# Kernel tuning notes

Measured on AMD Instinct MI355X. Metric: run time of the kernel, lower is better.

The kernel has to match this reference:

```python
import jax, jax.numpy as jnp
import numpy as np

N_EMBD = 512
N_HEADS = 8
N_KV_HEADS = 2
HEAD_DIM = N_EMBD // N_HEADS  # 64
ROPE_BASE = 1000000.0
B, T = 2, 4096


def _rotate_half(x):
    h = x.shape[-1] // 2
    return jnp.concatenate([-x[..., h:], x[..., :h]], axis=-1)


def _build_rope(head_dim, seq_len, base, dtype):
    inv_freq = 1.0 / base ** (jnp.arange(0, head_dim, 2, dtype=jnp.float32) / head_dim)
    t = jnp.arange(seq_len, dtype=jnp.float32)
    freqs = jnp.outer(t, inv_freq)            # [T, head_dim/2]
    emb = jnp.concatenate([freqs, freqs], axis=-1)  # [T, head_dim]
    return emb.astype(dtype), None  # placeholder, cos/sin computed by caller


def setup_inputs() -> dict:
    key = jax.random.key(0)
    ks = jax.random.split(key, 8)
    s_in = 1.0 / np.sqrt(N_EMBD)
    x = jax.random.normal(ks[0], (B, T, N_EMBD), dtype=jnp.float32)
    Wq = jax.random.normal(ks[1], (N_EMBD, N_HEADS * HEAD_DIM), dtype=jnp.float32) * s_in
    bq = jnp.zeros((N_HEADS * HEAD_DIM,), dtype=jnp.float32)
    Wk = jax.random.normal(ks[2], (N_EMBD, N_KV_HEADS * HEAD_DIM), dtype=jnp.float32) * s_in
    bk = jnp.zeros((N_KV_HEADS * HEAD_DIM,), dtype=jnp.float32)
    Wv = jax.random.normal(ks[3], (N_EMBD, N_KV_HEADS * HEAD_DIM), dtype=jnp.float32) * s_in
    bv = jnp.zeros((N_KV_HEADS * HEAD_DIM,), dtype=jnp.float32)
    Wo = jax.random.normal(ks[4], (N_HEADS * HEAD_DIM, N_EMBD), dtype=jnp.float32) * s_in
    return {"x": x, "Wq": Wq, "bq": bq, "Wk": Wk, "bk": bk, "Wv": Wv, "bv": bv, "Wo": Wo}


def reference(x, Wq, bq, Wk, bk, Wv, bv, Wo):
    Bx, Tx, _ = x.shape
    scale = HEAD_DIM ** -0.5
    q = (x @ Wq + bq).reshape(Bx, Tx, N_HEADS, HEAD_DIM).transpose(0, 2, 1, 3)      # [B,H,T,D]
    k = (x @ Wk + bk).reshape(Bx, Tx, N_KV_HEADS, HEAD_DIM).transpose(0, 2, 1, 3)   # [B,Hkv,T,D]
    v = (x @ Wv + bv).reshape(Bx, Tx, N_KV_HEADS, HEAD_DIM).transpose(0, 2, 1, 3)

    # RoPE (built in fp32 then cast, matching torch impl)
    inv_freq = 1.0 / ROPE_BASE ** (jnp.arange(0, HEAD_DIM, 2, dtype=jnp.float32) / HEAD_DIM)
    t = jnp.arange(Tx, dtype=jnp.float32)
    freqs = jnp.outer(t, inv_freq)
    emb = jnp.concatenate([freqs, freqs], axis=-1)          # [T, D]
    cos = jnp.cos(emb).astype(x.dtype)[None, None, :, :]    # broadcast over B,H
    sin = jnp.sin(emb).astype(x.dtype)[None, None, :, :]
    q = q * cos + _rotate_half(q) * sin
    k = k * cos + _rotate_half(k) * sin

    rep = N_HEADS // N_KV_HEADS
    k = jnp.repeat(k, rep, axis=1)   # repeat_interleave on head dim
    v = jnp.repeat(v, rep, axis=1)

    attn = jnp.einsum("bhtd,bhsd->bhts", q, k) * scale      # [B,H,T,T]
    causal = jnp.tril(jnp.ones((Tx, Tx), dtype=bool))
    attn = jnp.where(causal, attn, jnp.finfo(attn.dtype).min)
    attn = jax.nn.softmax(attn, axis=-1)
    out = jnp.einsum("bhts,bhsd->bhtd", attn, v)            # [B,H,T,D]
    out = out.transpose(0, 2, 1, 3).reshape(Bx, Tx, N_HEADS * HEAD_DIM)
    return out @ Wo
```

## Files before the change

kernel.cpp:

```cpp
#include <hip/hip_runtime.h>

typedef unsigned short u16;
typedef unsigned int u32;
typedef __bf16 bf16x8_t __attribute__((ext_vector_type(8)));
typedef float f32x4_t __attribute__((ext_vector_type(4)));
typedef float f32x16_t __attribute__((ext_vector_type(16)));

#define T_SEQ 4096
#define EMB 512
#define NH 8
#define NKV 2
#define HD 64

__device__ __forceinline__ float bf2f(u16 h) {
    union { unsigned u; float f; } x; x.u = ((unsigned)h) << 16; return x.f;
}
__device__ __forceinline__ u16 f2bf(float f) {
    union { float f; unsigned u; } x; x.f = f;
    unsigned r = x.u + 0x7FFFu + ((x.u >> 16) & 1u);
    return (u16)(r >> 16);
}

__global__ void transpose_kernel(const float* __restrict__ W, u16* __restrict__ WT,
                                 int K, int N) {
    int i = blockIdx.x * 256 + threadIdx.x;
    if (i < K * N) {
        int n = i / K;
        int k = i - n * K;
        WT[i] = f2bf(W[(size_t)k * N + n]);
    }
}

__global__ void cvt_kernel(const float* __restrict__ in, u16* __restrict__ out, int n4) {
    int i = blockIdx.x * 256 + threadIdx.x;
    if (i < n4) {
        float4 v = *reinterpret_cast<const float4*>(in + (size_t)i * 4);
        u16 o[4] = { f2bf(v.x), f2bf(v.y), f2bf(v.z), f2bf(v.w) };
        *reinterpret_cast<uint2*>(out + (size_t)i * 4) = *reinterpret_cast<uint2*>(o);
    }
}

__global__ void rope_table_kernel(float* __restrict__ cost, float* __restrict__ sint) {
    int i = blockIdx.x * 256 + threadIdx.x;
    int t = i >> 5, j = i & 31;
    double invf = pow(1.0e6, -(double)j / 32.0);
    double ang = (double)t * invf;
    cost[i] = (float)cos(ang);
    sint[i] = (float)sin(ang);
}

template <int EPI>
__global__ __launch_bounds__(256)
void gemm_kernel(const u16* __restrict__ A, const u16* __restrict__ Bt, int K,
                 float* __restrict__ C, int N,
                 const float* __restrict__ bq, const float* __restrict__ bk,
                 const float* __restrict__ bv,
                 const float* __restrict__ cost, const float* __restrict__ sint,
                 u16* __restrict__ qw, u16* __restrict__ kw, u16* __restrict__ vt)
{
    __shared__ __align__(16) u16 As[128][72];
    __shared__ __align__(16) u16 Bs[128][72];

    const int tid  = threadIdx.x;
    const int lane = tid & 63, wave = tid >> 6;
    const int wr = wave >> 1, wc = wave & 1;
    const int tm = blockIdx.x, tn = blockIdx.y;
    const int lrow = lane & 15, lgrp = lane >> 4;

    f32x4_t acc[4][4];
#pragma unroll
    for (int i = 0; i < 4; ++i)
#pragma unroll
        for (int j = 0; j < 4; ++j) acc[i][j] = (f32x4_t){0.f, 0.f, 0.f, 0.f};

    for (int k0 = 0; k0 < K; k0 += 64) {
        __syncthreads();
        {
            const int r0 = tid >> 3;
            const int ko = (tid & 7) * 8;
#pragma unroll
            for (int rr = 0; rr < 4; ++rr) {
                int row = r0 + rr * 32;
                uint4 va = *reinterpret_cast<const uint4*>(A + (size_t)(tm * 128 + row) * K + k0 + ko);
                *reinterpret_cast<uint4*>(&As[row][ko]) = va;
                uint4 vb = *reinterpret_cast<const uint4*>(Bt + (size_t)(tn * 128 + row) * K + k0 + ko);
                *reinterpret_cast<uint4*>(&Bs[row][ko]) = vb;
            }
        }
        __syncthreads();
#pragma unroll
        for (int kc = 0; kc < 2; ++kc) {
            bf16x8_t af[4], bf[4];
#pragma unroll
            for (int mb = 0; mb < 4; ++mb)
                af[mb] = *reinterpret_cast<const bf16x8_t*>(&As[wr * 64 + mb * 16 + lrow][kc * 32 + lgrp * 8]);
#pragma unroll
            for (int nb = 0; nb < 4; ++nb)
                bf[nb] = *reinterpret_cast<const bf16x8_t*>(&Bs[wc * 64 + nb * 16 + lrow][kc * 32 + lgrp * 8]);
#pragma unroll
            for (int mb = 0; mb < 4; ++mb)
#pragma unroll
                for (int nb = 0; nb < 4; ++nb)
                    acc[mb][nb] = __builtin_amdgcn_mfma_f32_16x16x32_bf16(af[mb], bf[nb], acc[mb][nb], 0, 0, 0);
        }
    }

    if (EPI == 0) {
#pragma unroll
        for (int mb = 0; mb < 4; ++mb)
#pragma unroll
            for (int nb = 0; nb < 4; ++nb)
#pragma unroll
                for (int r = 0; r < 4; ++r) {
                    int row = tm * 128 + wr * 64 + mb * 16 + lgrp * 4 + r;
                    int col = tn * 128 + wc * 64 + nb * 16 + lrow;
                    C[(size_t)row * N + col] = acc[mb][nb][r];
                }
    } else {
        const float QSC = 0.125f * 1.44269504088896f;
#pragma unroll
        for (int mb = 0; mb < 4; ++mb)
#pragma unroll
            for (int r = 0; r < 4; ++r) {
                int grow = tm * 128 + wr * 64 + mb * 16 + lgrp * 4 + r;
                int b = grow >> 12, t = grow & 4095;
#pragma unroll
                for (int nb = 0; nb < 2; ++nb) {
                    int n = tn * 128 + wc * 64 + nb * 16 + lrow;
                    int j = n & 63;
                    float c0 = acc[mb][nb][r];
                    float c1 = acc[mb][nb + 2][r];
                    if (n < 512) {
                        c0 += bq[n]; c1 += bq[n + 32];
                        float cs = cost[t * 32 + j], sn = sint[t * 32 + j];
                        float r0 = (c0 * cs - c1 * sn) * QSC;
                        float r1 = (c1 * cs + c0 * sn) * QSC;
                        int h = n >> 6;
                        size_t base = ((size_t)(b * NH + h) * T_SEQ + t) * HD;
                        qw[base + j]      = f2bf(r0);
                        qw[base + j + 32] = f2bf(r1);
                    } else if (n < 640) {
                        int nn = n - 512;
                        c0 += bk[nn]; c1 += bk[nn + 32];
                        float cs = cost[t * 32 + j], sn = sint[t * 32 + j];
                        float r0 = c0 * cs - c1 * sn;
                        float r1 = c1 * cs + c0 * sn;
                        int hk2 = nn >> 6;
                        size_t base = ((size_t)(b * NKV + hk2) * T_SEQ + t) * HD;
                        kw[base + j]      = f2bf(r0);
                        kw[base + j + 32] = f2bf(r1);
                    } else {
                        int nn = n - 640;
                        c0 += bv[nn]; c1 += bv[nn + 32];
                        int hv = nn >> 6;
                        size_t base = (size_t)(b * NKV + hv) * HD * T_SEQ;
                        vt[base + (size_t)j * T_SEQ + t]        = f2bf(c0);
                        vt[base + (size_t)(j + 32) * T_SEQ + t] = f2bf(c1);
                    }
                }
            }
    }
}

__global__ __launch_bounds__(256)
void attn_kernel(const u16* __restrict__ qw, const u16* __restrict__ kw,
                 const u16* __restrict__ vt, u16* __restrict__ po0,
                 u16* __restrict__ po12, float* __restrict__ lb)
{
    __shared__ __align__(16) u16 Ks[2][64][64];
    __shared__ __align__(16) u16 Vs[2][64][64];

    int gid = blockIdx.x;
    int qt = 31, nt, nc;
    for (;;) {
        nt = 2 * qt + 2;
        nc = (nt + 21) / 22;
        int g = nc * 16;
        if (gid < g) break;
        gid -= g; --qt;
    }
    const int bh = gid / nc;
    const int ck = gid - bh * nc;
    const int b = bh >> 3, h = bh & 7, hk = h >> 2;
    const int kt0 = ck * nt / nc;
    const int kt1 = (ck + 1) * nt / nc;

    const int tid = threadIdx.x, lane = tid & 63, wave = tid >> 6;
    const int lid = lane & 31, hi = lane >> 5;
    const int q0 = qt * 128 + wave * 32;

    const u16* kbase  = kw + (size_t)(b * NKV + hk) * T_SEQ * HD;
    const u16* vtbase = vt + (size_t)(b * NKV + hk) * HD * T_SEQ;

    const int ss = tid >> 3;
    const int sg = tid & 7;
    const int swz = (sg ^ (ss & 7)) << 3;

    bf16x8_t qf[4];
    {
        const u16* qrow = qw + ((size_t)(b * NH + h) * T_SEQ + q0 + lid) * HD + 8 * hi;
#pragma unroll
        for (int t = 0; t < 4; ++t)
            qf[t] = *reinterpret_cast<const bf16x8_t*>(qrow + 16 * t);
    }

    f32x16_t o0, o1;
#pragma unroll
    for (int i = 0; i < 16; ++i) { o0[i] = 0.f; o1[i] = 0.f; }
    const float M_FIX = 16.0f;
    float l = 0.f;

    {
        const int s2 = kt0 * 64;
        uint4 ka  = *reinterpret_cast<const uint4*>(kbase + (size_t)(s2 + ss) * HD + sg * 8);
        uint4 kb2 = *reinterpret_cast<const uint4*>(kbase + (size_t)(s2 + ss + 32) * HD + sg * 8);
        uint4 va  = *reinterpret_cast<const uint4*>(vtbase + (size_t)ss * T_SEQ + s2 + sg * 8);
        uint4 vb2 = *reinterpret_cast<const uint4*>(vtbase + (size_t)(ss + 32) * T_SEQ + s2 + sg * 8);
        *reinterpret_cast<uint4*>(&Ks[0][ss][swz]) = ka;
        *reinterpret_cast<uint4*>(&Ks[0][ss + 32][swz]) = kb2;
        *reinterpret_cast<uint4*>(&Vs[0][ss][swz]) = va;
        *reinterpret_cast<uint4*>(&Vs[0][ss + 32][swz]) = vb2;
    }
    __syncthreads();

    for (int kt = kt0; kt < kt1; ++kt) {
        const int cur = (kt - kt0) & 1, nxt = cur ^ 1;
        const bool pre = (kt + 1 < kt1);

        uint4 kr0, kr1, vr0, vr1;
        if (pre) {
            const int s2 = (kt + 1) * 64;
            kr0 = *reinterpret_cast<const uint4*>(kbase + (size_t)(s2 + ss) * HD + sg * 8);
            kr1 = *reinterpret_cast<const uint4*>(kbase + (size_t)(s2 + ss + 32) * HD + sg * 8);
            vr0 = *reinterpret_cast<const uint4*>(vtbase + (size_t)ss * T_SEQ + s2 + sg * 8);
            vr1 = *reinterpret_cast<const uint4*>(vtbase + (size_t)(ss + 32) * T_SEQ + s2 + sg * 8);
        }

        if (kt * 64 <= q0 + 31) {
            const bool full = (kt * 64 + 32 <= q0 + 31);
            const bool mreq = (kt * 64 + 63 > q0);

            f32x16_t s0, s1;
#pragma unroll
            for (int i = 0; i < 16; ++i) { s0[i] = 0.f; s1[i] = 0.f; }
            __builtin_amdgcn_s_setprio(1);
#pragma unroll
            for (int t = 0; t < 4; ++t) {
                const int g = ((2 * t + hi) ^ (lid & 7)) << 3;
                bf16x8_t ka = *reinterpret_cast<const bf16x8_t*>(&Ks[cur][lid][g]);
                s0 = __builtin_amdgcn_mfma_f32_32x32x16_bf16(ka, qf[t], s0, 0, 0, 0);
                if (full) {
                    bf16x8_t kb2 = *reinterpret_cast<const bf16x8_t*>(&Ks[cur][lid + 32][g]);
                    s1 = __builtin_amdgcn_mfma_f32_32x32x16_bf16(kb2, qf[t], s1, 0, 0, 0);
                }
            }
            __builtin_amdgcn_s_setprio(0);

            if (mreq) {
                const int qg = q0 + lid;
                const int kvb = kt * 64 + 4 * hi;
#pragma unroll
                for (int r = 0; r < 16; ++r) {
                    int kv = kvb + (r & 3) + 8 * (r >> 2);
                    if (kv > qg) s0[r] = -1e30f;
                    if (full && kv + 32 > qg) s1[r] = -1e30f;
                }
            }

#pragma unroll
            for (int r = 0; r < 16; ++r) s0[r] = exp2f(s0[r] - M_FIX);
            if (full) {
#pragma unroll
                for (int r = 0; r < 16; ++r) s1[r] = exp2f(s1[r] - M_FIX);
            }

            {
                float rs = 0.f;
#pragma unroll
                for (int q4 = 0; q4 < 4; ++q4)
                    rs += (s0[4 * q4] + s0[4 * q4 + 1]) + (s0[4 * q4 + 2] + s0[4 * q4 + 3]);
                if (full) {
#pragma unroll
                    for (int q4 = 0; q4 < 4; ++q4)
                        rs += (s1[4 * q4] + s1[4 * q4 + 1]) + (s1[4 * q4 + 2] + s1[4 * q4 + 3]);
                }
                rs += __shfl_xor(rs, 32);
                l += rs;
            }

            bf16x8_t pa[4];
            {
                u32 pw[8], pe[8];
                uint4 f0, f1;
#pragma unroll
                for (int c = 0; c < 4; ++c) {
                    asm("v_cvt_pk_bf16_f32 %0, %1, %2" : "=v"(pw[2 * c])     : "v"(s0[4 * c]),     "v"(s0[4 * c + 1]));
                    asm("v_cvt_pk_bf16_f32 %0, %1, %2" : "=v"(pw[2 * c + 1]) : "v"(s0[4 * c + 2]), "v"(s0[4 * c + 3]));
                }
#pragma unroll
                for (int i = 0; i < 8; ++i) pe[i] = (u32)__shfl_xor((int)pw[i], 32);
                f0.x = hi ? pe[2] : pw[0]; f0.y = hi ? pe[3] : pw[1];
                f0.z = hi ? pw[2] : pe[0]; f0.w = hi ? pw[3] : pe[1];
                f1.x = hi ? pe[6] : pw[4]; f1.y = hi ? pe[7] : pw[5];
                f1.z = hi ? pw[6] : pe[4]; f1.w = hi ? pw[7] : pe[5];
                pa[0] = __builtin_bit_cast(bf16x8_t, f0);
                pa[1] = __builtin_bit_cast(bf16x8_t, f1);
                if (full) {
#pragma unroll
                    for (int c = 0; c < 4; ++c) {
                        asm("v_cvt_pk_bf16_f32 %0, %1, %2" : "=v"(pw[2 * c])     : "v"(s1[4 * c]),     "v"(s1[4 * c + 1]));
                        asm("v_cvt_pk_bf16_f32 %0, %1, %2" : "=v"(pw[2 * c + 1]) : "v"(s1[4 * c + 2]), "v"(s1[4 * c + 3]));
                    }
#pragma unroll
                    for (int i = 0; i < 8; ++i) pe[i] = (u32)__shfl_xor((int)pw[i], 32);
                    f0.x = hi ? pe[2] : pw[0]; f0.y = hi ? pe[3] : pw[1];
                    f0.z = hi ? pw[2] : pe[0]; f0.w = hi ? pw[3] : pe[1];
                    f1.x = hi ? pe[6] : pw[4]; f1.y = hi ? pe[7] : pw[5];
                    f1.z = hi ? pw[6] : pe[4]; f1.w = hi ? pw[7] : pe[5];
                    pa[2] = __builtin_bit_cast(bf16x8_t, f0);
                    pa[3] = __builtin_bit_cast(bf16x8_t, f1);
                }
            }

            __builtin_amdgcn_s_setprio(1);
            const int ns = full ? 4 : 2;
#pragma unroll
            for (int s = 0; s < 4; ++s) {
                if (s >= ns) break;
                const int g = ((2 * s + hi) ^ (lid & 7)) << 3;
                bf16x8_t v0f = *reinterpret_cast<const bf16x8_t*>(&Vs[cur][lid][g]);
                bf16x8_t v1f = *reinterpret_cast<const bf16x8_t*>(&Vs[cur][lid + 32][g]);
                o0 = __builtin_amdgcn_mfma_f32_32x32x16_bf16(pa[s], v0f, o0, 0, 0, 0);
                o1 = __builtin_amdgcn_mfma_f32_32x32x16_bf16(pa[s], v1f, o1, 0, 0, 0);
            }
            __builtin_amdgcn_s_setprio(0);
        }

        if (pre) {
            *reinterpret_cast<uint4*>(&Ks[nxt][ss][swz]) = kr0;
            *reinterpret_cast<uint4*>(&Ks[nxt][ss + 32][swz]) = kr1;
            *reinterpret_cast<uint4*>(&Vs[nxt][ss][swz]) = vr0;
            *reinterpret_cast<uint4*>(&Vs[nxt][ss + 32][swz]) = vr1;
            __syncthreads();
        }
    }

    {
        u16* pob = (ck == 0) ? po0 : (po12 + (size_t)(ck - 1) * 4194304);
        const int rowb = (bh * 32 + qt) * 128 + wave * 32;
#pragma unroll
        for (int r = 0; r < 16; ++r) {
            int qr = (r & 3) + 8 * (r >> 2) + 4 * hi;
            size_t base = (size_t)(rowb + qr) * HD;
            pob[base + lid]      = f2bf(o0[r]);
            pob[base + lid + 32] = f2bf(o1[r]);
        }
        if (hi == 0)
            lb[(size_t)ck * 65536 + rowb + lid] = l;
    }
}

__global__ __launch_bounds__(256)
void combine_kernel(const u16* __restrict__ po0, const u16* __restrict__ po12,
                    const float* __restrict__ lb, u16* __restrict__ ao)
{
    int id = blockIdx.x * 256 + threadIdx.x;
    int row = id >> 3, oct = id & 7;
    int bhqt = row >> 7, qrow = row & 127;
    int bh = bhqt >> 5, qt = bhqt & 31;
    int b = bh >> 3, h = bh & 7;
    int t = qt * 128 + qrow;
    int nc = (2 * qt + 2 + 21) / 22;

    float lsum = lb[row];
    if (nc > 1) lsum += lb[65536 + row];
    if (nc > 2) lsum += lb[131072 + row];
    float inv = 1.0f / lsum;

    float acc[8];
    {
        uint4 a = *reinterpret_cast<const uint4*>(po0 + (size_t)row * HD + oct * 8);
        const u16* pa = reinterpret_cast<const u16*>(&a);
#pragma unroll
        for (int j = 0; j < 8; ++j) acc[j] = bf2f(pa[j]);
    }
    if (nc > 1) {
        uint4 a = *reinterpret_cast<const uint4*>(po12 + (size_t)row * HD + oct * 8);
        const u16* pa = reinterpret_cast<const u16*>(&a);
#pragma unroll
        for (int j = 0; j < 8; ++j) acc[j] += bf2f(pa[j]);
    }
    if (nc > 2) {
        uint4 a = *reinterpret_cast<const uint4*>(po12 + 4194304 + (size_t)row * HD + oct * 8);
        const u16* pa = reinterpret_cast<const u16*>(&a);
#pragma unroll
        for (int j = 0; j < 8; ++j) acc[j] += bf2f(pa[j]);
    }

    u16 outv[8];
#pragma unroll
    for (int j = 0; j < 8; ++j) outv[j] = f2bf(acc[j] * inv);
    size_t base = ((size_t)(b * T_SEQ) + t) * EMB + h * HD + oct * 8;
    *reinterpret_cast<uint2*>(ao + base)     = *reinterpret_cast<uint2*>(&outv[0]);
    *reinterpret_cast<uint2*>(ao + base + 4) = *reinterpret_cast<uint2*>(&outv[4]);
}

extern "C" void kernel_launch(void* const* d_in, const int* in_sizes, int n_in,
                              void* d_out, int out_size, void* d_ws, size_t ws_size,
                              hipStream_t stream)
{
    const float* x  = (const float*)d_in[0];
    const float* Wq = (const float*)d_in[1];
    const float* bq = (const float*)d_in[2];
    const float* Wk = (const float*)d_in[3];
    const float* bk = (const float*)d_in[4];
    const float* Wv = (const float*)d_in[5];
    const float* bv = (const float*)d_in[6];
    const float* Wo = (const float*)d_in[7];
    float* out = (float*)d_out;

    char* ws = (char*)d_ws;
    u16*   WqkvT = (u16*)(ws);
    u16*   WoT   = (u16*)(ws + 786432);
    float* cost  = (float*)(ws + 1310720);
    float* sint  = (float*)(ws + 1835008);
    u16*   xbf   = (u16*)(ws + 2359296);
    u16*   qw    = (u16*)(ws + 10747904);
    u16*   kw    = (u16*)(ws + 19136512);
    u16*   vt    = (u16*)(ws + 21233664);
    u16*   ao    = (u16*)(ws + 23330816);
    u16*   po0   = xbf;
    u16*   po12  = (u16*)(ws + 31719424);
    float* lb    = (float*)(ws + 48496640);

    transpose_kernel<<<(512 * 512 + 255) / 256, 256, 0, stream>>>(Wq, WqkvT, 512, 512);
    transpose_kernel<<<(512 * 128 + 255) / 256, 256, 0, stream>>>(Wk, WqkvT + 512 * 512, 512, 128);
    transpose_kernel<<<(512 * 128 + 255) / 256, 256, 0, stream>>>(Wv, WqkvT + 640 * 512, 512, 128);
    transpose_kernel<<<(512 * 512 + 255) / 256, 256, 0, stream>>>(Wo, WoT, 512, 512);
    cvt_kernel<<<(2 * T_SEQ * EMB / 4 + 255) / 256, 256, 0, stream>>>(x, xbf, 2 * T_SEQ * EMB / 4);
    rope_table_kernel<<<(T_SEQ * 32) / 256, 256, 0, stream>>>(cost, sint);

    dim3 gp(64, 6);
    gemm_kernel<1><<<gp, 256, 0, stream>>>(xbf, WqkvT, 512, nullptr, 768,
                                           bq, bk, bv, cost, sint, qw, kw, vt);

    attn_kernel<<<1008, 256, 0, stream>>>(qw, kw, vt, po0, po12, lb);

    combine_kernel<<<65536 * 8 / 256, 256, 0, stream>>>(po0, po12, lb, ao);

    dim3 go(64, 4);
    gemm_kernel<0><<<go, 256, 0, stream>>>(ao, WoT, 512, out, 512,
                                           nullptr, nullptr, nullptr, nullptr, nullptr,
                                           nullptr, nullptr, nullptr);
}
```

Baseline: 161.3 us.

## Interleave head index in block mapping and use permlane32 swap for P repack

```diff
diff --git a/kernel.cpp b/kernel.cpp
--- a/kernel.cpp
+++ b/kernel.cpp
@@ -170,21 +170,20 @@
     __shared__ __align__(16) u16 Ks[2][64][64];
     __shared__ __align__(16) u16 Vs[2][64][64];
 
-    int gid = blockIdx.x;
-    int qt = 31, nt, nc;
+    const int hdix = blockIdx.x & 15;
+    int s = blockIdx.x >> 4;
+    int qt = 31, nc;
     for (;;) {
-        nt = 2 * qt + 2;
-        nc = (nt + 21) / 22;
-        int g = nc * 16;
-        if (gid < g) break;
-        gid -= g; --qt;
-    }
-    const int bh = gid / nc;
-    const int ck = gid - bh * nc;
-    const int b = bh >> 3, h = bh & 7, hk = h >> 2;
+        nc = (2 * qt + 23) / 22;
+        if (s < nc) break;
+        s -= nc; --qt;
+    }
+    const int ck = s;
+    const int nt = 2 * qt + 2;
     const int kt0 = ck * nt / nc;
     const int kt1 = (ck + 1) * nt / nc;
 
+    const int b = hdix >> 3, h = hdix & 7, hk = h >> 2;
     const int tid = threadIdx.x, lane = tid & 63, wave = tid >> 6;
     const int lid = lane & 31, hi = lane >> 5;
     const int q0 = qt * 128 + wave * 32;
@@ -204,9 +203,9 @@
             qf[t] = *reinterpret_cast<const bf16x8_t*>(qrow + 16 * t);
     }
 
-    f32x16_t o0, o1;
-#pragma unroll
-    for (int i = 0; i < 16; ++i) { o0[i] = 0.f; o1[i] = 0.f; }
+    f32x16_t o0, o1, z16;
+#pragma unroll
+    for (int i = 0; i < 16; ++i) { o0[i] = 0.f; o1[i] = 0.f; z16[i] = 0.f; }
     const float M_FIX = 16.0f;
     float l = 0.f;
 
@@ -241,17 +240,15 @@
             const bool mreq = (kt * 64 + 63 > q0);
 
             f32x16_t s0, s1;
-#pragma unroll
-            for (int i = 0; i < 16; ++i) { s0[i] = 0.f; s1[i] = 0.f; }
             __builtin_amdgcn_s_setprio(1);
 #pragma unroll
             for (int t = 0; t < 4; ++t) {
                 const int g = ((2 * t + hi) ^ (lid & 7)) << 3;
                 bf16x8_t ka = *reinterpret_cast<const bf16x8_t*>(&Ks[cur][lid][g]);
-                s0 = __builtin_amdgcn_mfma_f32_32x32x16_bf16(ka, qf[t], s0, 0, 0, 0);
+                s0 = __builtin_amdgcn_mfma_f32_32x32x16_bf16(ka, qf[t], (t == 0) ? z16 : s0, 0, 0, 0);
                 if (full) {
                     bf16x8_t kb2 = *reinterpret_cast<const bf16x8_t*>(&Ks[cur][lid + 32][g]);
-                    s1 = __builtin_amdgcn_mfma_f32_32x32x16_bf16(kb2, qf[t], s1, 0, 0, 0);
+                    s1 = __builtin_amdgcn_mfma_f32_32x32x16_bf16(kb2, qf[t], (t == 0) ? z16 : s1, 0, 0, 0);
                 }
             }
             __builtin_amdgcn_s_setprio(0);
@@ -290,19 +287,18 @@
 
             bf16x8_t pa[4];
             {
-                u32 pw[8], pe[8];
-                uint4 f0, f1;
+                u32 pw[8];
 #pragma unroll
                 for (int c = 0; c < 4; ++c) {
                     asm("v_cvt_pk_bf16_f32 %0, %1, %2" : "=v"(pw[2 * c])     : "v"(s0[4 * c]),     "v"(s0[4 * c + 1]));
                     asm("v_cvt_pk_bf16_f32 %0, %1, %2" : "=v"(pw[2 * c + 1]) : "v"(s0[4 * c + 2]), "v"(s0[4 * c + 3]));
                 }
-#pragma unroll
-                for (int i = 0; i < 8; ++i) pe[i] = (u32)__shfl_xor((int)pw[i], 32);
-                f0.x = hi ? pe[2] : pw[0]; f0.y = hi ? pe[3] : pw[1];
-                f0.z = hi ? pw[2] : pe[0]; f0.w = hi ? pw[3] : pe[1];
-                f1.x = hi ? pe[6] : pw[4]; f1.y = hi ? pe[7] : pw[5];
-                f1.z = hi ? pw[6] : pe[4]; f1.w = hi ? pw[7] : pe[5];
+                asm("v_permlane32_swap_b32 %0, %1" : "+v"(pw[0]), "+v"(pw[2]));
+                asm("v_permlane32_swap_b32 %0, %1" : "+v"(pw[1]), "+v"(pw[3]));
+                asm("v_permlane32_swap_b32 %0, %1" : "+v"(pw[4]), "+v"(pw[6]));
+                asm("v_permlane32_swap_b32 %0, %1" : "+v"(pw[5]), "+v"(pw[7]));
+                uint4 f0 = {pw[0], pw[1], pw[2], pw[3]};
+                uint4 f1 = {pw[4], pw[5], pw[6], pw[7]};
                 pa[0] = __builtin_bit_cast(bf16x8_t, f0);
                 pa[1] = __builtin_bit_cast(bf16x8_t, f1);
                 if (full) {
@@ -311,27 +307,27 @@
                         asm("v_cvt_pk_bf16_f32 %0, %1, %2" : "=v"(pw[2 * c])     : "v"(s1[4 * c]),     "v"(s1[4 * c + 1]));
                         asm("v_cvt_pk_bf16_f32 %0, %1, %2" : "=v"(pw[2 * c + 1]) : "v"(s1[4 * c + 2]), "v"(s1[4 * c + 3]));
                     }
-#pragma unroll
-                    for (int i = 0; i < 8; ++i) pe[i] = (u32)__shfl_xor((int)pw[i], 32);
-                    f0.x = hi ? pe[2] : pw[0]; f0.y = hi ? pe[3] : pw[1];
-                    f0.z = hi ? pw[2] : pe[0]; f0.w = hi ? pw[3] : pe[1];
-                    f1.x = hi ? pe[6] : pw[4]; f1.y = hi ? pe[7] : pw[5];
-                    f1.z = hi ? pw[6] : pe[4]; f1.w = hi ? pw[7] : pe[5];
-                    pa[2] = __builtin_bit_cast(bf16x8_t, f0);
-                    pa[3] = __builtin_bit_cast(bf16x8_t, f1);
+                    asm("v_permlane32_swap_b32 %0, %1" : "+v"(pw[0]), "+v"(pw[2]));
+                    asm("v_permlane32_swap_b32 %0, %1" : "+v"(pw[1]), "+v"(pw[3]));
+                    asm("v_permlane32_swap_b32 %0, %1" : "+v"(pw[4]), "+v"(pw[6]));
+                    asm("v_permlane32_swap_b32 %0, %1" : "+v"(pw[5]), "+v"(pw[7]));
+                    uint4 g0 = {pw[0], pw[1], pw[2], pw[3]};
+                    uint4 g1 = {pw[4], pw[5], pw[6], pw[7]};
+                    pa[2] = __builtin_bit_cast(bf16x8_t, g0);
+                    pa[3] = __builtin_bit_cast(bf16x8_t, g1);
                 }
             }
 
             __builtin_amdgcn_s_setprio(1);
             const int ns = full ? 4 : 2;
 #pragma unroll
-            for (int s = 0; s < 4; ++s) {
-                if (s >= ns) break;
-                const int g = ((2 * s + hi) ^ (lid & 7)) << 3;
+            for (int s2 = 0; s2 < 4; ++s2) {
+                if (s2 >= ns) break;
+                const int g = ((2 * s2 + hi) ^ (lid & 7)) << 3;
                 bf16x8_t v0f = *reinterpret_cast<const bf16x8_t*>(&Vs[cur][lid][g]);
                 bf16x8_t v1f = *reinterpret_cast<const bf16x8_t*>(&Vs[cur][lid + 32][g]);
-                o0 = __builtin_amdgcn_mfma_f32_32x32x16_bf16(pa[s], v0f, o0, 0, 0, 0);
-                o1 = __builtin_amdgcn_mfma_f32_32x32x16_bf16(pa[s], v1f, o1, 0, 0, 0);
+                o0 = __builtin_amdgcn_mfma_f32_32x32x16_bf16(pa[s2], v0f, o0, 0, 0, 0);
+                o1 = __builtin_amdgcn_mfma_f32_32x32x16_bf16(pa[s2], v1f, o1, 0, 0, 0);
             }
             __builtin_amdgcn_s_setprio(0);
         }
@@ -347,7 +343,7 @@
 
     {
         u16* pob = (ck == 0) ? po0 : (po12 + (size_t)(ck - 1) * 4194304);
-        const int rowb = (bh * 32 + qt) * 128 + wave * 32;
+        const int rowb = (hdix * 32 + qt) * 128 + wave * 32;
 #pragma unroll
         for (int r = 0; r < 16; ++r) {
             int qr = (r & 3) + 8 * (r >> 2) + 4 * hi;
@@ -370,7 +366,7 @@
     int bh = bhqt >> 5, qt = bhqt & 31;
     int b = bh >> 3, h = bh & 7;
     int t = qt * 128 + qrow;
-    int nc = (2 * qt + 2 + 21) / 22;
+    int nc = (2 * qt + 23) / 22;
 
     float lsum = lb[row];
     if (nc > 1) lsum += lb[65536 + row];
```

Measured after the change: 155.7 us. 3.5% less time.
